# Kernel tuning notes

Hardware: AMD Instinct MI355X
Metric: run time of the kernel (lower is better)

The kernel has to match this reference:

```python
import jax, jax.numpy as jnp
import numpy as np

B, C, L = 2048, 9605, 8
ALPHA = 0.5        # self.alpha
ALPHA1 = 0.05      # margin
ALPHA2 = 2.0       # asymmetric scale when violated
ALPHA3 = 5.0       # logistic sharpness
ALPHA_OTHER = 0.3  # floor on top-k threshold
TOPK = 16          # x_sorted[15] -> 16th largest


def setup_inputs() -> dict:
    key = jax.random.key(0)
    k1, k2, k3, k4 = jax.random.split(key, 4)
    x = jax.random.normal(k1, (B, C), dtype=jnp.float32)
    # each class assigned to one of 5*L slots; slots < L are whitelist groups,
    # the rest are 'other' classes (like total_indices in the torch code)
    gid = jax.random.randint(k4, (C,), 0, 5 * L)
    gid = gid.at[:L].set(jnp.arange(L))  # guarantee every group is non-empty
    group_mask = gid[None, :] == jnp.arange(L)[:, None]  # [L, C] bool
    # sparse multi-label binarized targets (~14 positives/sample)
    y = (jax.random.uniform(k2, (B, C)) < 0.0015).astype(jnp.float32)
    y_neg = (jax.random.uniform(k3, (B, C)) < 0.0015).astype(jnp.float32)
    return {"x": x, "y": y, "y_neg": y_neg, "group_mask": group_mask}


def _rank_loss(x1, x2):
    # our_rank_loss: sigmoid(alpha3*(x2-x1+margin)), scaled by alpha2 when violated
    d = x2 - x1 + ALPHA1
    s = jax.nn.sigmoid(ALPHA3 * d)
    return jnp.where(d > 0, ALPHA2 * s, s)


def reference(x, y, y_neg, group_mask):
    xs = jax.nn.sigmoid(x)  # [B, C]
    # top_k_thres = max(16th-largest sigmoid score, alpha_other)
    thres = jnp.maximum(jax.lax.top_k(xs, TOPK)[0][:, TOPK - 1], ALPHA_OTHER)  # [B]
    maskf = group_mask.astype(xs.dtype)  # [L, C]
    neg_inf = jnp.array(-jnp.inf, xs.dtype)
    # per-sample max score inside each whitelist group: [B, L]
    group_max = jnp.max(jnp.where(group_mask[None, :, :], xs[:, None, :], neg_inf), axis=-1)
    # find_gt_whitelist: group is 'hit' if any positive target inside it
    gt = (y @ maskf.T) > 0        # [B, L]
    gt_neg = (y_neg @ maskf.T) > 0  # [B, L]
    has_gt = jnp.any(gt, axis=-1)    # [B]; False <=> sentinel len(all_labels)
    has_neg = jnp.any(gt_neg, axis=-1)
    # ---- case B: sample hits at least one whitelist group ----
    rl_correct = _rank_loss(group_max, thres[:, None])    # gt groups above thres
    rl_incorrect = _rank_loss(thres[:, None], group_max)  # non-gt groups below thres
    caseB = jnp.sum(jnp.where(gt, rl_correct, rl_incorrect), axis=-1)  # [B]
    # ---- case A: no whitelist group hit ----
    union = jnp.any(group_mask, axis=0)  # [C] union of all whitelist classes
    union_max = jnp.max(jnp.where(union[None, :], xs, neg_inf), axis=-1)  # [B]
    neg_max = jnp.max(jnp.where(gt_neg, group_max, neg_inf), axis=-1)
    neg_score = jnp.where(has_neg, neg_max, jnp.zeros((), xs.dtype))  # torch starts at 0
    caseA = (1.0 - ALPHA) * _rank_loss(thres, union_max) + ALPHA * _rank_loss(thres, neg_score)
    loss_rank_all = jnp.where(has_gt, caseB, caseA)  # [B]
    return jnp.mean(loss_rank_all)
```

## Files before the change

### kernel.cpp

```cpp
#include <hip/hip_runtime.h>
#include <math.h>

constexpr int B_ = 2048;
constexpr int C_ = 9605;
constexpr int L_ = 8;
constexpr int TOPK_ = 16;
constexpr int CAP_ = 512;
constexpr float T0_ = 2.0f;
constexpr int GSEG_ = 512;

typedef float vfloat4 __attribute__((ext_vector_type(4)));

__device__ __forceinline__ float sigm(float v) { return 1.0f / (1.0f + expf(-v)); }

__device__ __forceinline__ float rank_loss(float x1, float x2) {
  float d = x2 - x1 + 0.05f;
  float s = 1.0f / (1.0f + expf(-5.0f * d));
  return (d > 0.0f) ? 2.0f * s : s;
}

__device__ __forceinline__ unsigned int fkey(float v) {
  unsigned int u = __float_as_uint(v);
  return u ^ ((u & 0x80000000u) ? 0xFFFFFFFFu : 0x80000000u);
}
__device__ __forceinline__ float fkeyinv(unsigned int k) {
  unsigned int u = (k & 0x80000000u) ? (k ^ 0x80000000u) : ~k;
  return __uint_as_float(u);
}

__global__ void build_code_kernel(const int* __restrict__ mask,
                                  unsigned char* __restrict__ code) {
  int c = blockIdx.x * 256 + threadIdx.x;
  if (c >= C_) return;
  unsigned char cd = 0xFF;
#pragma unroll
  for (int l = L_ - 1; l >= 0; --l)
    if (mask[l * C_ + c] != 0) cd = (unsigned char)l;
  code[c] = cd;
}

__global__ void build_glist_kernel(const unsigned char* __restrict__ code,
                                   unsigned int* __restrict__ glist) {
  __shared__ int cnt;
  __shared__ unsigned int firstidx;
  const int l = blockIdx.x;
  const int t = threadIdx.x;
  if (t == 0) { cnt = 0; firstidx = 0u; }
  __syncthreads();
  for (int c = t; c < C_; c += 256) {
    if (code[c] == (unsigned char)l) {
      int p = atomicAdd(&cnt, 1);
      if (p < GSEG_) glist[l * GSEG_ + p] = (unsigned int)c;
      if (p == 0) firstidx = (unsigned int)c;
    }
  }
  __syncthreads();
  int n = (cnt < GSEG_) ? cnt : GSEG_;
  unsigned int f = firstidx;
  for (int s = n + t; s < GSEG_; s += 256) glist[l * GSEG_ + s] = f;
}

__global__ void __launch_bounds__(256) row_loss_kernel(
    const float* __restrict__ x, const float* __restrict__ y,
    const float* __restrict__ yn, const unsigned char* __restrict__ code,
    const unsigned int* __restrict__ glist, float* __restrict__ loss) {
  __shared__ float cand[CAP_];
  __shared__ int cand_cnt;
  __shared__ float wgm[4][L_];
  __shared__ unsigned int wgt[4], wgn[4];
  __shared__ float s_x16;
  __shared__ int s_red;

  const int t = threadIdx.x;
  const int b = blockIdx.x;
  const size_t rb = (size_t)b * C_;
  const float* xr = x + rb;
  const float* yr = y + rb;
  const float* nr = yn + rb;
  if (t == 0) cand_cnt = 0;
  __syncthreads();

  unsigned int gtb = 0u, gnb = 0u;

  auto cappend = [&](float v) {
    int p = atomicAdd(&cand_cnt, 1);
    if (p < CAP_) cand[p] = v;
  };
  auto candq = [&](vfloat4 v) {
    float m = fmaxf(fmaxf(v.x, v.y), fmaxf(v.z, v.w));
    if (m > T0_) {
      if (v.x > T0_) cappend(v.x);
      if (v.y > T0_) cappend(v.y);
      if (v.z > T0_) cappend(v.z);
      if (v.w > T0_) cappend(v.w);
    }
  };
  auto posq = [&](vfloat4 v, int c0, unsigned int& bits) {
    float m = fmaxf(fmaxf(v.x, v.y), fmaxf(v.z, v.w));
    if (m > 0.0f) {
      if (v.x > 0.0f) { unsigned char cd = code[c0];     if (cd < L_) bits |= 1u << cd; }
      if (v.y > 0.0f) { unsigned char cd = code[c0 + 1]; if (cd < L_) bits |= 1u << cd; }
      if (v.z > 0.0f) { unsigned char cd = code[c0 + 2]; if (cd < L_) bits |= 1u << cd; }
      if (v.w > 0.0f) { unsigned char cd = code[c0 + 3]; if (cd < L_) bits |= 1u << cd; }
    }
  };
  auto scalar_elem = [&](int c) {
    float v = xr[c];
    if (v > T0_) cappend(v);
    if (yr[c] > 0.0f) { unsigned char cd = code[c]; if (cd < L_) gtb |= 1u << cd; }
    if (nr[c] > 0.0f) { unsigned char cd = code[c]; if (cd < L_) gnb |= 1u << cd; }
  };

  const int lead = (4 - (b & 3)) & 3;
  const int n4 = (C_ - lead) >> 2;
  const vfloat4* x4 = reinterpret_cast<const vfloat4*>(x) + ((rb + lead) >> 2);
  const vfloat4* y4 = reinterpret_cast<const vfloat4*>(y) + ((rb + lead) >> 2);
  const vfloat4* v4 = reinterpret_cast<const vfloat4*>(yn) + ((rb + lead) >> 2);

  for (int kb = 0; kb < 2048; kb += 1024) {
    int k0 = kb + t, k1 = k0 + 256, k2 = k0 + 512, k3 = k0 + 768;
    vfloat4 a0 = __builtin_nontemporal_load(x4 + k0);
    vfloat4 a1 = __builtin_nontemporal_load(x4 + k1);
    vfloat4 a2 = __builtin_nontemporal_load(x4 + k2);
    vfloat4 a3 = __builtin_nontemporal_load(x4 + k3);
    vfloat4 b0 = __builtin_nontemporal_load(y4 + k0);
    vfloat4 b1 = __builtin_nontemporal_load(y4 + k1);
    vfloat4 b2 = __builtin_nontemporal_load(y4 + k2);
    vfloat4 b3 = __builtin_nontemporal_load(y4 + k3);
    vfloat4 c0 = __builtin_nontemporal_load(v4 + k0);
    vfloat4 c1 = __builtin_nontemporal_load(v4 + k1);
    vfloat4 c2 = __builtin_nontemporal_load(v4 + k2);
    vfloat4 c3 = __builtin_nontemporal_load(v4 + k3);
    candq(a0); candq(a1); candq(a2); candq(a3);
    posq(b0, lead + 4 * k0, gtb); posq(b1, lead + 4 * k1, gtb);
    posq(b2, lead + 4 * k2, gtb); posq(b3, lead + 4 * k3, gtb);
    posq(c0, lead + 4 * k0, gnb); posq(c1, lead + 4 * k1, gnb);
    posq(c2, lead + 4 * k2, gnb); posq(c3, lead + 4 * k3, gnb);
  }
  for (int k = 2048 + t; k < n4; k += 256) {
    vfloat4 a = __builtin_nontemporal_load(x4 + k);
    vfloat4 bq = __builtin_nontemporal_load(y4 + k);
    vfloat4 cq = __builtin_nontemporal_load(v4 + k);
    candq(a);
    posq(bq, lead + 4 * k, gtb);
    posq(cq, lead + 4 * k, gnb);
  }
  if (t < lead) scalar_elem(t);
  const int ts = lead + (n4 << 2);
  if (t >= 64 && t < 64 + (C_ - ts)) scalar_elem(ts + (t - 64));

  float gm[L_];
#pragma unroll
  for (int l = 0; l < L_; ++l) {
    unsigned int ia = glist[l * GSEG_ + t];
    unsigned int ib = glist[l * GSEG_ + 256 + t];
    gm[l] = fmaxf(xr[ia], xr[ib]);
  }

#pragma unroll
  for (int off = 32; off > 0; off >>= 1) {
#pragma unroll
    for (int l = 0; l < L_; ++l) gm[l] = fmaxf(gm[l], __shfl_xor(gm[l], off, 64));
    gtb |= (unsigned int)__shfl_xor((int)gtb, off, 64);
    gnb |= (unsigned int)__shfl_xor((int)gnb, off, 64);
  }
  if ((t & 63) == 0) {
    int w = t >> 6;
#pragma unroll
    for (int l = 0; l < L_; ++l) wgm[w][l] = gm[l];
    wgt[w] = gtb;
    wgn[w] = gnb;
  }
  __syncthreads();

  const int cnt = cand_cnt;
  const bool mainp = (cnt >= TOPK_) && (cnt <= CAP_);
  if (mainp) {
    if (t < 64) {
      unsigned int ku[CAP_ / 64];
#pragma unroll
      for (int k = 0; k < CAP_ / 64; ++k) {
        int idx = t + (k << 6);
        ku[k] = (idx < cnt) ? fkey(cand[idx]) : 0u;
      }
      unsigned int lo = 0u, hi = 0xFFFFFFFFu;
      for (int it = 0; it < 32 && lo < hi; ++it) {
        unsigned int mid = lo + ((hi - lo) >> 1) + 1u;
        int c16 = 0;
#pragma unroll
        for (int k = 0; k < CAP_ / 64; ++k) c16 += (ku[k] >= mid) ? 1 : 0;
#pragma unroll
        for (int off = 32; off > 0; off >>= 1) c16 += __shfl_xor(c16, off, 64);
        if (c16 >= TOPK_) lo = mid; else hi = mid - 1u;
      }
      if (t == 0) s_x16 = fkeyinv(lo);
    }
  } else {
    unsigned int lo = 0u, hi = 0xFFFFFFFFu;
    for (int it = 0; it < 32; ++it) {
      if (lo >= hi) break;
      unsigned int mid = lo + ((hi - lo) >> 1) + 1u;
      if (t == 0) s_red = 0;
      __syncthreads();
      int cl = 0;
      for (int c = t; c < C_; c += 256) cl += (fkey(xr[c]) >= mid) ? 1 : 0;
      atomicAdd(&s_red, cl);
      __syncthreads();
      int total = s_red;
      __syncthreads();
      if (total >= TOPK_) lo = mid; else hi = mid - 1u;
    }
    if (t == 0) s_x16 = fkeyinv(lo);
  }
  __syncthreads();

  if (t == 0) {
    float thres = fmaxf(sigm(s_x16), 0.3f);
    unsigned int gtbf = wgt[0] | wgt[1] | wgt[2] | wgt[3];
    unsigned int gnbf = wgn[0] | wgn[1] | wgn[2] | wgn[3];
    float caseB = 0.0f, unio = -INFINITY, negmax = -INFINITY;
#pragma unroll
    for (int l = 0; l < L_; ++l) {
      float gx = fmaxf(fmaxf(wgm[0][l], wgm[1][l]), fmaxf(wgm[2][l], wgm[3][l]));
      float g = sigm(gx);
      unio = fmaxf(unio, g);
      caseB += ((gtbf >> l) & 1u) ? rank_loss(g, thres) : rank_loss(thres, g);
      if ((gnbf >> l) & 1u) negmax = fmaxf(negmax, g);
    }
    float negscore = (gnbf != 0u) ? negmax : 0.0f;
    float caseA = 0.5f * rank_loss(thres, unio) + 0.5f * rank_loss(thres, negscore);
    loss[b] = (gtbf != 0u) ? caseB : caseA;
  }
}

__global__ void mean_kernel(const float* __restrict__ loss, float* __restrict__ out) {
  const int t = threadIdx.x;
  float s = 0.0f;
  for (int i = t; i < B_; i += 256) s += loss[i];
#pragma unroll
  for (int off = 32; off > 0; off >>= 1) s += __shfl_xor(s, off, 64);
  __shared__ float part[4];
  if ((t & 63) == 0) part[t >> 6] = s;
  __syncthreads();
  if (t == 0) out[0] = (part[0] + part[1] + part[2] + part[3]) * (1.0f / (float)B_);
}

extern "C" void kernel_launch(void* const* d_in, const int* in_sizes, int n_in,
                              void* d_out, int out_size, void* d_ws, size_t ws_size,
                              hipStream_t stream) {
  const float* x = (const float*)d_in[0];
  const float* y = (const float*)d_in[1];
  const float* yn = (const float*)d_in[2];
  const int* mask = (const int*)d_in[3];

  char* ws = (char*)d_ws;
  float* loss = (float*)ws;
  unsigned char* code = (unsigned char*)(ws + 8192);
  unsigned int* glist = (unsigned int*)(ws + 8192 + 9632);

  hipLaunchKernelGGL(build_code_kernel, dim3((C_ + 255) / 256), dim3(256), 0, stream,
                     mask, code);
  hipLaunchKernelGGL(build_glist_kernel, dim3(L_), dim3(256), 0, stream,
                     code, glist);
  hipLaunchKernelGGL(row_loss_kernel, dim3(B_), dim3(256), 0, stream,
                     x, y, yn, code, glist, loss);
  hipLaunchKernelGGL(mean_kernel, dim3(1), dim3(256), 0, stream,
                     loss, (float*)d_out);
}
```

Before: 262.5 us.

## Issue all row loads up front, raise candidate threshold, fuse mean via atomics

The main streaming loop becomes a fully unrolled load phase: 6 plus 4 guarded vfloat4 loads per thread for x, y and y_neg are all issued before any processing, and plain loads replace the nontemporal ones. The candidate threshold rises from 2.0 to 2.45 and the candidate buffer shrinks from 512 to 128 entries, cutting shared-memory appends. The separate mean kernel is removed; each block adds its scaled loss to the output with an atomic after a memset. This adds a threshold assumption that depends on the input distribution (enough values above 2.45 to find the 16th largest), and the atomic sum makes the result order-nondeterministic.

```diff
diff --git a/kernel.cpp b/kernel.cpp
--- a/kernel.cpp
+++ b/kernel.cpp
@@ -5,8 +5,8 @@
 constexpr int C_ = 9605;
 constexpr int L_ = 8;
 constexpr int TOPK_ = 16;
-constexpr int CAP_ = 512;
-constexpr float T0_ = 2.0f;
+constexpr int CAP_ = 128;
+constexpr float T0_ = 2.45f;
 constexpr int GSEG_ = 512;
 
 typedef float vfloat4 __attribute__((ext_vector_type(4)));
@@ -63,7 +63,7 @@
 __global__ void __launch_bounds__(256) row_loss_kernel(
     const float* __restrict__ x, const float* __restrict__ y,
     const float* __restrict__ yn, const unsigned char* __restrict__ code,
-    const unsigned int* __restrict__ glist, float* __restrict__ loss) {
+    const unsigned int* __restrict__ glist, float* __restrict__ out) {
   __shared__ float cand[CAP_];
   __shared__ int cand_cnt;
   __shared__ float wgm[4][L_];
@@ -117,33 +117,46 @@
   const vfloat4* y4 = reinterpret_cast<const vfloat4*>(y) + ((rb + lead) >> 2);
   const vfloat4* v4 = reinterpret_cast<const vfloat4*>(yn) + ((rb + lead) >> 2);
 
-  for (int kb = 0; kb < 2048; kb += 1024) {
-    int k0 = kb + t, k1 = k0 + 256, k2 = k0 + 512, k3 = k0 + 768;
-    vfloat4 a0 = __builtin_nontemporal_load(x4 + k0);
-    vfloat4 a1 = __builtin_nontemporal_load(x4 + k1);
-    vfloat4 a2 = __builtin_nontemporal_load(x4 + k2);
-    vfloat4 a3 = __builtin_nontemporal_load(x4 + k3);
-    vfloat4 b0 = __builtin_nontemporal_load(y4 + k0);
-    vfloat4 b1 = __builtin_nontemporal_load(y4 + k1);
-    vfloat4 b2 = __builtin_nontemporal_load(y4 + k2);
-    vfloat4 b3 = __builtin_nontemporal_load(y4 + k3);
-    vfloat4 c0 = __builtin_nontemporal_load(v4 + k0);
-    vfloat4 c1 = __builtin_nontemporal_load(v4 + k1);
-    vfloat4 c2 = __builtin_nontemporal_load(v4 + k2);
-    vfloat4 c3 = __builtin_nontemporal_load(v4 + k3);
-    candq(a0); candq(a1); candq(a2); candq(a3);
-    posq(b0, lead + 4 * k0, gtb); posq(b1, lead + 4 * k1, gtb);
-    posq(b2, lead + 4 * k2, gtb); posq(b3, lead + 4 * k3, gtb);
-    posq(c0, lead + 4 * k0, gnb); posq(c1, lead + 4 * k1, gnb);
-    posq(c2, lead + 4 * k2, gnb); posq(c3, lead + 4 * k3, gnb);
-  }
-  for (int k = 2048 + t; k < n4; k += 256) {
-    vfloat4 a = __builtin_nontemporal_load(x4 + k);
-    vfloat4 bq = __builtin_nontemporal_load(y4 + k);
-    vfloat4 cq = __builtin_nontemporal_load(v4 + k);
-    candq(a);
-    posq(bq, lead + 4 * k, gtb);
-    posq(cq, lead + 4 * k, gnb);
+  {
+    vfloat4 xa[6], ya[6], na[6];
+#pragma unroll
+    for (int i = 0; i < 6; ++i) xa[i] = x4[t + 256 * i];
+#pragma unroll
+    for (int i = 0; i < 6; ++i) ya[i] = y4[t + 256 * i];
+#pragma unroll
+    for (int i = 0; i < 6; ++i) na[i] = v4[t + 256 * i];
+#pragma unroll
+    for (int i = 0; i < 6; ++i) {
+      int k = t + 256 * i;
+      candq(xa[i]);
+      posq(ya[i], lead + 4 * k, gtb);
+      posq(na[i], lead + 4 * k, gnb);
+    }
+  }
+  {
+    int kk[4];
+    bool act[4];
+#pragma unroll
+    for (int i = 0; i < 4; ++i) {
+      int k = t + 256 * (6 + i);
+      act[i] = (k < n4);
+      kk[i] = act[i] ? k : (n4 - 1);
+    }
+    vfloat4 xa[4], ya[4], na[4];
+#pragma unroll
+    for (int i = 0; i < 4; ++i) xa[i] = x4[kk[i]];
+#pragma unroll
+    for (int i = 0; i < 4; ++i) ya[i] = y4[kk[i]];
+#pragma unroll
+    for (int i = 0; i < 4; ++i) na[i] = v4[kk[i]];
+#pragma unroll
+    for (int i = 0; i < 4; ++i) {
+      if (act[i]) {
+        candq(xa[i]);
+        posq(ya[i], lead + 4 * kk[i], gtb);
+        posq(na[i], lead + 4 * kk[i], gnb);
+      }
+    }
   }
   if (t < lead) scalar_elem(t);
   const int ts = lead + (n4 << 2);
@@ -229,20 +242,9 @@
     }
     float negscore = (gnbf != 0u) ? negmax : 0.0f;
     float caseA = 0.5f * rank_loss(thres, unio) + 0.5f * rank_loss(thres, negscore);
-    loss[b] = (gtbf != 0u) ? caseB : caseA;
-  }
-}
-
-__global__ void mean_kernel(const float* __restrict__ loss, float* __restrict__ out) {
-  const int t = threadIdx.x;
-  float s = 0.0f;
-  for (int i = t; i < B_; i += 256) s += loss[i];
-#pragma unroll
-  for (int off = 32; off > 0; off >>= 1) s += __shfl_xor(s, off, 64);
-  __shared__ float part[4];
-  if ((t & 63) == 0) part[t >> 6] = s;
-  __syncthreads();
-  if (t == 0) out[0] = (part[0] + part[1] + part[2] + part[3]) * (1.0f / (float)B_);
+    float lb = (gtbf != 0u) ? caseB : caseA;
+    atomicAdd(out, lb * (1.0f / (float)B_));
+  }
 }
 
 extern "C" void kernel_launch(void* const* d_in, const int* in_sizes, int n_in,
@@ -254,16 +256,14 @@
   const int* mask = (const int*)d_in[3];
 
   char* ws = (char*)d_ws;
-  float* loss = (float*)ws;
-  unsigned char* code = (unsigned char*)(ws + 8192);
-  unsigned int* glist = (unsigned int*)(ws + 8192 + 9632);
-
+  unsigned char* code = (unsigned char*)ws;
+  unsigned int* glist = (unsigned int*)(ws + 9632);
+
+  hipMemsetAsync(d_out, 0, sizeof(float), stream);
   hipLaunchKernelGGL(build_code_kernel, dim3((C_ + 255) / 256), dim3(256), 0, stream,
                      mask, code);
   hipLaunchKernelGGL(build_glist_kernel, dim3(L_), dim3(256), 0, stream,
                      code, glist);
   hipLaunchKernelGGL(row_loss_kernel, dim3(B_), dim3(256), 0, stream,
-                     x, y, yn, code, glist, loss);
-  hipLaunchKernelGGL(mean_kernel, dim3(1), dim3(256), 0, stream,
-                     loss, (float*)d_out);
-}
+                     x, y, yn, code, glist, (float*)d_out);
+}
```

Result: slower. 277.7 us (+5.8%).
